# Kernel optimization log

Measured on AMD Instinct MI355X. Metric: run time of the kernel, lower is better.

Reference implementation:

```python
import jax, jax.numpy as jnp
import numpy as np

B, N = 16, 16          # batch, boxes per image
H, W = 640, 640        # image size
PH, PW = 300, 300      # learned patch size
MIN_AREA = 60.0
MAX_ANG = 20.0 * np.pi / 180.0


def setup_inputs() -> dict:
    key = jax.random.key(0)
    k1, k2, k3 = jax.random.split(key, 3)
    images = jax.random.uniform(k1, (B, H, W, 3), jnp.float32, -1.0, 1.0)
    patch = jax.random.uniform(k2, (PH, PW, 3), jnp.float32, -1.0, 1.0)
    kb1, kb2, kb3 = jax.random.split(k3, 3)
    ymin = jax.random.uniform(kb1, (B, N), jnp.float32, 0.0, H - 220.0)
    xmin = jax.random.uniform(kb2, (B, N), jnp.float32, 0.0, W - 220.0)
    hw = jax.random.uniform(kb3, (B, N, 2), jnp.float32, 100.0, 200.0)
    boxes = jnp.stack([ymin, xmin, ymin + hw[..., 0], xmin + hw[..., 1]], axis=-1)
    scale = jnp.float32(0.4)
    return {"boxes": boxes, "images": images, "patch": patch, "scale": scale}


def _bilinear(img, ys, xs):
    # img [Ph,Pw,3]; ys,xs [H,W] continuous source coords -> [H,W,3]
    Ph, Pw = img.shape[0], img.shape[1]
    y0 = jnp.floor(ys)
    x0 = jnp.floor(xs)
    wy = (ys - y0)[..., None]
    wx = (xs - x0)[..., None]
    y0i = jnp.clip(y0.astype(jnp.int32), 0, Ph - 1)
    y1i = jnp.clip(y0i + 1, 0, Ph - 1)
    x0i = jnp.clip(x0.astype(jnp.int32), 0, Pw - 1)
    x1i = jnp.clip(x0i + 1, 0, Pw - 1)
    v00 = img[y0i, x0i]
    v01 = img[y0i, x1i]
    v10 = img[y1i, x0i]
    v11 = img[y1i, x1i]
    return v00 * (1 - wy) * (1 - wx) + v01 * (1 - wy) * wx + v10 * wy * (1 - wx) + v11 * wy * wx


def _per_image(img, boxes_i, patch, scale, key):
    # random_print_adjust: per-channel affine jitter of the patch
    kw, kb, kloop = jax.random.split(key, 3)
    w = jax.random.normal(kw, (1, 1, 3), jnp.float32) * 0.1 + 0.5
    b = jax.random.normal(kb, (1, 1, 3), jnp.float32) * 0.01
    p = jnp.clip(w * patch + b, -1.0, 1.0)
    # BrightnessMatcher: shift patch mean brightness to match the image
    p = jnp.clip(p + (jnp.mean(img) - jnp.mean(p)), -1.0, 1.0)

    oimg = img
    mask0 = jnp.zeros_like(img)
    yy, xx = jnp.meshgrid(jnp.arange(H, dtype=jnp.float32),
                          jnp.arange(W, dtype=jnp.float32), indexing="ij")

    def step(carry, inp):
        image, mask = carry
        box, kk = inp
        ymin, xmin, ymax, xmax = box[0], box[1], box[2], box[3]
        h = ymax - ymin
        ww = xmax - xmin
        longer = jnp.maximum(h, ww)
        ps = jnp.floor(longer * scale)                       # patch_h == patch_w
        diag = jnp.minimum(jnp.sqrt(2.0).astype(jnp.float32) * ps, jnp.float32(W))
        oy = ymin + h / 2.0
        ox = xmin + ww / 2.0
        y0 = jnp.maximum(oy - diag / 2.0, 0.0)
        x0 = jnp.maximum(ox - diag / 2.0, 0.0)
        y0 = jnp.where(y0 + diag > H, H - diag, y0)
        x0 = jnp.where(x0 + diag > W, W - diag, x0)
        # int casts as in the TF code (values are >= 0, trunc == floor)
        y0i = jnp.floor(y0)
        x0i = jnp.floor(x0)
        phi = jnp.maximum(jnp.floor(ps), 1.0)
        diagi = jnp.floor(diag)
        valid_box = (phi * phi) > MIN_AREA

        k1, k2, k3 = jax.random.split(kk, 3)
        angle = jax.random.uniform(k1, (), jnp.float32, -MAX_ANG, MAX_ANG)

        # inverse warp: output pixel -> padded-patch coords -> resized-patch coords
        u = yy - y0i
        v = xx - x0i
        in_sq = (u >= 0) & (v >= 0) & (u < diagi) & (v < diagi)
        c = (diagi - 1.0) / 2.0
        ca, sa = jnp.cos(angle), jnp.sin(angle)
        su = c + ca * (u - c) - sa * (v - c)
        sv = c + sa * (u - c) + ca * (v - c)
        top = jnp.floor((diagi - phi) / 2.0)   # pad offset (floor top/left)
        py = su - top
        px = sv - top
        valid_src = (py >= 0) & (py <= phi - 1) & (px >= 0) & (px <= phi - 1)
        # resized-patch coords -> original patch coords (bilinear resize, half-pixel)
        sy = (py + 0.5) * (PH / phi) - 0.5
        sx = (px + 0.5) * (PW / phi) - 0.5
        samp = _bilinear(p, sy, sx)                                   # [H,W,3]
        noise = jax.random.uniform(k2, samp.shape, jnp.float32, -0.1, 0.1)
        bright = jax.random.uniform(k3, (), jnp.float32, -0.3, 0.3)
        im = jnp.clip(samp + noise + bright, -1.0, 1.0)
        val = jnp.where(valid_src[..., None], im, -2.0)
        val = jnp.where(val < -1.0, image, val)   # fill with current background
        val = jnp.clip(val, -1.0, 1.0)
        sel = (in_sq & valid_box)[..., None]
        new_image = jnp.where(sel, val, image)
        new_mask = jnp.where(sel, oimg - val, mask)
        return (new_image, new_mask), None

    keys = jax.random.split(kloop, N)
    (img_out, mask_out), _ = jax.lax.scan(step, (img, mask0), (boxes_i, keys))
    return img_out, mask_out


def reference(boxes, images, patch, scale):
    keys = jax.random.split(jax.random.key(42), B)
    img_out, mask_out = jax.vmap(_per_image, in_axes=(0, 0, None, None, 0))(
        images, boxes, patch, scale, keys)
    return img_out, mask_out
```

## Files before the change

### kernel.cpp

```cpp
#include <hip/hip_runtime.h>
#include <stdint.h>
#include <math.h>

#define B_ 16
#define N_ 16
#define H_ 640
#define W_ 640
#define PH_ 300
#define PW_ 300

#define IMG_ELEMS (H_*W_*3)
#define PATCH_ELEMS (PH_*PW_*3)

#define TROWS 16
#define TCOLS 64
#define TILES_Y (H_/TROWS)
#define TILES_X (W_/TCOLS)
#define TILES_PER_IMG (TILES_Y*TILES_X)

typedef float f32x4 __attribute__((ext_vector_type(4)));

__device__ __forceinline__ uint2 tf2x32(uint32_t k0, uint32_t k1, uint32_t x0, uint32_t x1) {
  uint32_t k2 = k0 ^ k1 ^ 0x1BD11BDAu;
#define TFR(r) x0 += x1; x1 = (x1 << (r)) | (x1 >> (32 - (r))); x1 ^= x0;
  x0 += k0; x1 += k1;
  TFR(13) TFR(15) TFR(26) TFR(6)
  x0 += k1; x1 += k2 + 1u;
  TFR(17) TFR(29) TFR(16) TFR(24)
  x0 += k2; x1 += k0 + 2u;
  TFR(13) TFR(15) TFR(26) TFR(6)
  x0 += k0; x1 += k1 + 3u;
  TFR(17) TFR(29) TFR(16) TFR(24)
  x0 += k1; x1 += k2 + 4u;
  TFR(13) TFR(15) TFR(26) TFR(6)
  x0 += k2; x1 += k0 + 5u;
#undef TFR
  return make_uint2(x0, x1);
}

__device__ __forceinline__ uint32_t rb32(uint32_t k0, uint32_t k1, uint32_t i) {
  uint2 o = tf2x32(k0, k1, 0u, i);
  return o.x ^ o.y;
}

__device__ __forceinline__ float u01f(uint32_t bits) {
  return __uint_as_float((bits >> 9) | 0x3F800000u) - 1.0f;
}

__device__ __forceinline__ float erfinv32(float x) {
  float w = -log1pf(-x * x);
  float p;
  if (w < 5.0f) {
    w = w - 2.5f;
    p = 2.81022636e-08f;
    p = fmaf(p, w, 3.43273939e-07f);
    p = fmaf(p, w, -3.5233877e-06f);
    p = fmaf(p, w, -4.39150654e-06f);
    p = fmaf(p, w, 0.00021858087f);
    p = fmaf(p, w, -0.00125372503f);
    p = fmaf(p, w, -0.00417768164f);
    p = fmaf(p, w, 0.246640727f);
    p = fmaf(p, w, 1.50140941f);
  } else {
    w = sqrtf(w) - 3.0f;
    p = -0.000200214257f;
    p = fmaf(p, w, 0.000100950558f);
    p = fmaf(p, w, 0.00134934322f);
    p = fmaf(p, w, -0.00367342844f);
    p = fmaf(p, w, 0.00573950773f);
    p = fmaf(p, w, -0.0076224613f);
    p = fmaf(p, w, 0.00943887047f);
    p = fmaf(p, w, 1.00167406f);
    p = fmaf(p, w, 2.83297682f);
  }
  return p * x;
}

__device__ __forceinline__ float jnormal(uint32_t bits) {
  float lo = __uint_as_float(0xBF7FFFFFu);
  float span = 1.0f - lo;
  float u = fmaxf(lo, u01f(bits) * span + lo);
  return 1.4142135623730951f * erfinv32(u);
}

__global__ void setup_kernel(const float* __restrict__ boxes, const float* __restrict__ scale_p,
                             float* __restrict__ params, float* __restrict__ wb) {
  int t = threadIdx.x;
  if (t >= B_*N_) return;
  int b = t >> 4, n = t & 15;
  uint2 kb = tf2x32(0u, 42u, 0u, (uint32_t)b);
  uint2 kw  = tf2x32(kb.x, kb.y, 0u, 0u);
  uint2 kbk = tf2x32(kb.x, kb.y, 0u, 1u);
  uint2 kl  = tf2x32(kb.x, kb.y, 0u, 2u);
  if (n == 0) {
    wb[b*8+0] = jnormal(rb32(kw.x,  kw.y,  0u)) * 0.1f + 0.5f;
    wb[b*8+1] = jnormal(rb32(kw.x,  kw.y,  1u)) * 0.1f + 0.5f;
    wb[b*8+2] = jnormal(rb32(kw.x,  kw.y,  2u)) * 0.1f + 0.5f;
    wb[b*8+3] = jnormal(rb32(kbk.x, kbk.y, 0u)) * 0.01f;
    wb[b*8+4] = jnormal(rb32(kbk.x, kbk.y, 1u)) * 0.01f;
    wb[b*8+5] = jnormal(rb32(kbk.x, kbk.y, 2u)) * 0.01f;
  }
  uint2 kk = tf2x32(kl.x, kl.y, 0u, (uint32_t)n);
  uint2 k1 = tf2x32(kk.x, kk.y, 0u, 0u);
  uint2 k2 = tf2x32(kk.x, kk.y, 0u, 1u);
  uint2 k3 = tf2x32(kk.x, kk.y, 0u, 2u);
  const float MA = (float)(20.0 * 3.14159265358979323846 / 180.0);
  float angle  = fmaxf(-MA,   u01f(rb32(k1.x, k1.y, 0u)) * (MA - (-MA)) + (-MA));
  float bright = fmaxf(-0.3f, u01f(rb32(k3.x, k3.y, 0u)) * (0.3f - (-0.3f)) + (-0.3f));

  const float* bx = boxes + (size_t)t * 4;
  float ymin = bx[0], xmin = bx[1], ymax = bx[2], xmax = bx[3];
  float sc = scale_p[0];
  float h = ymax - ymin, ww = xmax - xmin;
  float longer = fmaxf(h, ww);
  float ps = floorf(longer * sc);
  float diag = fminf(sqrtf(2.0f) * ps, (float)W_);
  float oy = ymin + h * 0.5f;
  float ox = xmin + ww * 0.5f;
  float y0 = fmaxf(oy - diag * 0.5f, 0.0f);
  float x0 = fmaxf(ox - diag * 0.5f, 0.0f);
  if (y0 + diag > (float)H_) y0 = (float)H_ - diag;
  if (x0 + diag > (float)W_) x0 = (float)W_ - diag;
  float y0i = floorf(y0), x0i = floorf(x0);
  float phi = fmaxf(floorf(ps), 1.0f);
  float diagi = floorf(diag);
  float validf = ((phi * phi) > 60.0f) ? 1.0f : 0.0f;
  float c = (diagi - 1.0f) * 0.5f;
  float top = floorf((diagi - phi) * 0.5f);

  float* P = params + t * 16;
  P[0] = y0i; P[1] = x0i; P[2] = diagi; P[3] = phi;
  P[4] = c;
  P[5] = (float)cos((double)angle);
  P[6] = (float)sin((double)angle);
  P[7] = top;
  P[8] = bright; P[9] = (float)PH_ / phi; P[10] = 0.0f; P[11] = validf;
  P[12] = __uint_as_float(k2.x); P[13] = __uint_as_float(k2.y); P[14] = 0.0f; P[15] = 0.0f;
}

__global__ __launch_bounds__(256) void reduce_kernel(
    const float* __restrict__ images, const float* __restrict__ patch,
    const float* __restrict__ wb, double* __restrict__ partials) {
  int b = blockIdx.y, j = blockIdx.x, t = threadIdx.x;
  const float* img = images + (size_t)b * IMG_ELEMS;
  double s = 0.0;
  for (int i = j * 256 + t; i < IMG_ELEMS; i += 64 * 256) s += (double)img[i];
  float w0 = wb[b*8+0], w1 = wb[b*8+1], w2 = wb[b*8+2];
  float b0 = wb[b*8+3], b1 = wb[b*8+4], b2 = wb[b*8+5];
  double sp = 0.0;
  for (int i = j * 256 + t; i < PATCH_ELEMS; i += 64 * 256) {
    int q = i / 3; int ch = i - q * 3;
    float wv = (ch == 0) ? w0 : ((ch == 1) ? w1 : w2);
    float bv = (ch == 0) ? b0 : ((ch == 1) ? b1 : b2);
    float pv = fminf(fmaxf(wv * patch[i] + bv, -1.0f), 1.0f);
    sp += (double)pv;
  }
  __shared__ double sh[256];
  sh[t] = s; __syncthreads();
  for (int o = 128; o > 0; o >>= 1) { if (t < o) sh[t] += sh[t + o]; __syncthreads(); }
  if (t == 0) partials[((size_t)b * 64 + j) * 2 + 0] = sh[0];
  __syncthreads();
  sh[t] = sp; __syncthreads();
  for (int o = 128; o > 0; o >>= 1) { if (t < o) sh[t] += sh[t + o]; __syncthreads(); }
  if (t == 0) partials[((size_t)b * 64 + j) * 2 + 1] = sh[0];
}

__global__ void finalize_kernel(const double* __restrict__ partials, float* __restrict__ dvals) {
  int t = threadIdx.x;
  if (t < B_) {
    double si = 0.0, sp = 0.0;
    for (int j = 0; j < 64; j++) {
      si += partials[((size_t)t * 64 + j) * 2 + 0];
      sp += partials[((size_t)t * 64 + j) * 2 + 1];
    }
    float mi = (float)(si / (double)IMG_ELEMS);
    float mp = (float)(sp / (double)PATCH_ELEMS);
    dvals[t] = mi - mp;
  }
}

__global__ __launch_bounds__(256) void patch_adjust_kernel(
    const float* __restrict__ patch, const float* __restrict__ wb,
    const float* __restrict__ dvals, float* __restrict__ padj) {
  int b = blockIdx.y;
  float w0 = wb[b*8+0], w1 = wb[b*8+1], w2 = wb[b*8+2];
  float b0 = wb[b*8+3], b1 = wb[b*8+4], b2 = wb[b*8+5];
  float dsh = dvals[b];
  float* dst = padj + (size_t)b * PATCH_ELEMS;
  int i0 = (blockIdx.x * 256 + threadIdx.x) * 4;
  if (i0 + 4 <= PATCH_ELEMS) {
    f32x4 pv = *(const f32x4*)(patch + i0);
    float o[4];
#pragma unroll
    for (int e = 0; e < 4; e++) {
      int ch = (i0 + e) % 3;
      float wv = (ch == 0) ? w0 : ((ch == 1) ? w1 : w2);
      float bv = (ch == 0) ? b0 : ((ch == 1) ? b1 : b2);
      float a = fminf(fmaxf(wv * pv[e] + bv, -1.0f), 1.0f);
      o[e] = fminf(fmaxf(a + dsh, -1.0f), 1.0f);
    }
    f32x4 ov = {o[0], o[1], o[2], o[3]};
    *(f32x4*)(dst + i0) = ov;
  }
}

template<int PADJ>
__global__ __launch_bounds__(256) void main_kernel(
    const float* __restrict__ images, const float* __restrict__ patchsrc,
    const float* __restrict__ params, const float* __restrict__ wb,
    const float* __restrict__ dvals, float* __restrict__ out) {
  __shared__ float sP[N_ * 16];
  __shared__ float sWB[6];
  __shared__ int sList[N_];
  __shared__ int sCount;
  __shared__ float sT[TROWS * 192];

  int bid = blockIdx.x;
  int b  = (bid & 7) * 2 + ((bid >> 3) & 1);
  int tl = bid >> 4;
  int ty = tl / TILES_X;
  int tx = tl - ty * TILES_X;
  int tid = threadIdx.x;

  if (tid < N_ * 16) sP[tid] = params[b * N_ * 16 + tid];
  if (PADJ == 0 && tid < 6) sWB[tid] = wb[b * 8 + tid];
  if (tid == 0) {
    const float* Pb = params + b * N_ * 16;
    float ys = (float)(ty * TROWS), ye = (float)(ty * TROWS + TROWS - 1);
    float xs = (float)(tx * TCOLS), xe = (float)(tx * TCOLS + TCOLS - 1);
    int cnt = 0;
    for (int n = 0; n < N_; n++) {
      const float* P = Pb + n * 16;
      if (P[11] == 0.0f) continue;
      float last = P[2] - 1.0f;
      if (P[0] + last < ys || P[0] > ye) continue;
      if (P[1] + last < xs || P[1] > xe) continue;
      sList[cnt++] = n;
    }
    sCount = cnt;
  }
  __syncthreads();

  int lane = tid & 63;
  int wv   = tid >> 6;
  size_t ibase = (size_t)b * IMG_ELEMS;
  size_t moff  = (size_t)B_ * IMG_ELEMS;

  int   ck[3], lrk[3];
  size_t fbk[3];
#pragma unroll
  for (int k = 0; k < 3; k++) {
    int t4 = k * 64 + lane;
    int r  = t4 / 48;
    int c  = t4 - r * 48;
    int lr = wv * 4 + r;
    ck[k] = c; lrk[k] = lr;
    fbk[k] = ibase + ((size_t)(ty * TROWS + lr) * W_ + tx * TCOLS) * 3 + (size_t)c * 4;
  }

  if (sCount == 0) {
    const f32x4 z = {0.0f, 0.0f, 0.0f, 0.0f};
#pragma unroll
    for (int k = 0; k < 3; k++) {
      f32x4 d = *(const f32x4*)(images + fbk[k]);
      __builtin_nontemporal_store(d, (f32x4*)(out + fbk[k]));
      __builtin_nontemporal_store(z, (f32x4*)(out + moff + fbk[k]));
    }
    return;
  }

  const float* patchb = PADJ ? (patchsrc + (size_t)b * PATCH_ELEMS) : patchsrc;
  float dsh = PADJ ? 0.0f : dvals[b];

#pragma unroll
  for (int k = 0; k < 3; k++) {
    f32x4 d = *(const f32x4*)(images + fbk[k]);
    *(f32x4*)(&sT[lrk[k] * 192 + ck[k] * 4]) = d;
  }

  int   pj[4];  float yfj[4];
  float xf = (float)(tx * TCOLS + lane);
#pragma unroll
  for (int j = 0; j < 4; j++) {
    int row = ty * TROWS + wv * 4 + j;
    pj[j]  = row * W_ + tx * TCOLS + lane;
    yfj[j] = (float)row;
  }

  float orig[12], img[12], mkv[12];
#pragma unroll
  for (int j = 0; j < 4; j++) {
    int base = (wv * 4 + j) * 192 + lane * 3;
    orig[j*3+0] = sT[base + 0];
    orig[j*3+1] = sT[base + 1];
    orig[j*3+2] = sT[base + 2];
  }
#pragma unroll
  for (int e = 0; e < 12; e++) { img[e] = orig[e]; mkv[e] = 0.0f; }

  int cnt = sCount;
  for (int li = 0; li < cnt; li++) {
    const float* P = sP + sList[li] * 16;
    float P0 = P[0], P1 = P[1], diagi = P[2];
    float phi = P[3], c = P[4], ca = P[5], sa = P[6], top = P[7], bright = P[8], sph = P[9];
    uint32_t k2a = __float_as_uint(P[12]);
    uint32_t k2b = __float_as_uint(P[13]);
    float v = xf - P1;
    bool vok = (v >= 0.0f && v < diagi);
    float t2 = v - c;
#pragma unroll
    for (int j = 0; j < 4; j++) {
      float u = yfj[j] - P0;
      if (!(u >= 0.0f && u < diagi)) continue;
      if (!vok) continue;
      float t1 = u - c;
      float su = (c + ca * t1) - sa * t2;
      float sv = (c + sa * t1) + ca * t2;
      float py = su - top;
      float px = sv - top;
      bool vsrc = (py >= 0.0f) && (py <= phi - 1.0f) && (px >= 0.0f) && (px <= phi - 1.0f);
      if (vsrc) {
        float sy = (py + 0.5f) * sph - 0.5f;
        float sx = (px + 0.5f) * sph - 0.5f;
        float fy = floorf(sy), fx = floorf(sx);
        float wy = sy - fy, wxv = sx - fx;
        int iy0 = min(max((int)fy, 0), PH_ - 1);
        int iy1 = min(iy0 + 1, PH_ - 1);
        int ix0 = min(max((int)fx, 0), PW_ - 1);
        int ix1 = min(ix0 + 1, PW_ - 1);
        int o00 = (iy0 * PW_ + ix0) * 3;
        int o01 = (iy0 * PW_ + ix1) * 3;
        int o10 = (iy1 * PW_ + ix0) * 3;
        int o11 = (iy1 * PW_ + ix1) * 3;
        float omwy = 1.0f - wy, omwx = 1.0f - wxv;
        int nbase = pj[j] * 3;
#pragma unroll
        for (int ch = 0; ch < 3; ch++) {
          float a00, a01, a10, a11;
          if (PADJ) {
            a00 = patchb[o00 + ch];
            a01 = patchb[o01 + ch];
            a10 = patchb[o10 + ch];
            a11 = patchb[o11 + ch];
          } else {
            float wv2 = sWB[ch], bv = sWB[3 + ch];
            a00 = fminf(fmaxf(wv2 * patchb[o00 + ch] + bv, -1.0f), 1.0f);
            a01 = fminf(fmaxf(wv2 * patchb[o01 + ch] + bv, -1.0f), 1.0f);
            a10 = fminf(fmaxf(wv2 * patchb[o10 + ch] + bv, -1.0f), 1.0f);
            a11 = fminf(fmaxf(wv2 * patchb[o11 + ch] + bv, -1.0f), 1.0f);
            a00 = fminf(fmaxf(a00 + dsh, -1.0f), 1.0f);
            a01 = fminf(fmaxf(a01 + dsh, -1.0f), 1.0f);
            a10 = fminf(fmaxf(a10 + dsh, -1.0f), 1.0f);
            a11 = fminf(fmaxf(a11 + dsh, -1.0f), 1.0f);
          }
          float samp = ((a00 * omwy) * omwx) + ((a01 * omwy) * wxv)
                     + ((a10 * wy) * omwx) + ((a11 * wy) * wxv);
          uint32_t bits = rb32(k2a, k2b, (uint32_t)(nbase + ch));
          float nz = fmaxf(-0.1f, u01f(bits) * (0.1f - (-0.1f)) + (-0.1f));
          float imv = fminf(fmaxf((samp + nz) + bright, -1.0f), 1.0f);
          img[j * 3 + ch] = imv;
          mkv[j * 3 + ch] = orig[j * 3 + ch] - imv;
        }
      } else {
#pragma unroll
        for (int ch = 0; ch < 3; ch++) mkv[j * 3 + ch] = orig[j * 3 + ch] - img[j * 3 + ch];
      }
    }
  }

#pragma unroll
  for (int j = 0; j < 4; j++) {
    int base = (wv * 4 + j) * 192 + lane * 3;
    sT[base + 0] = img[j*3+0];
    sT[base + 1] = img[j*3+1];
    sT[base + 2] = img[j*3+2];
  }
#pragma unroll
  for (int k = 0; k < 3; k++) {
    f32x4 d = *(const f32x4*)(&sT[lrk[k] * 192 + ck[k] * 4]);
    __builtin_nontemporal_store(d, (f32x4*)(out + fbk[k]));
  }
#pragma unroll
  for (int j = 0; j < 4; j++) {
    int base = (wv * 4 + j) * 192 + lane * 3;
    sT[base + 0] = mkv[j*3+0];
    sT[base + 1] = mkv[j*3+1];
    sT[base + 2] = mkv[j*3+2];
  }
#pragma unroll
  for (int k = 0; k < 3; k++) {
    f32x4 d = *(const f32x4*)(&sT[lrk[k] * 192 + ck[k] * 4]);
    __builtin_nontemporal_store(d, (f32x4*)(out + moff + fbk[k]));
  }
}

extern "C" void kernel_launch(void* const* d_in, const int* in_sizes, int n_in,
                              void* d_out, int out_size, void* d_ws, size_t ws_size,
                              hipStream_t stream) {
  const float* boxes  = (const float*)d_in[0];
  const float* images = (const float*)d_in[1];
  const float* patch  = (const float*)d_in[2];
  const float* scale  = (const float*)d_in[3];
  float* out = (float*)d_out;

  float* params = (float*)d_ws;
  float* wb     = params + B_ * N_ * 16;
  float* dvals  = wb + B_ * 8;
  double* partials = (double*)((char*)d_ws + 20480);
  float* padj   = (float*)((char*)d_ws + 36864);
  const size_t PADJ_NEED = 36864 + (size_t)B_ * PATCH_ELEMS * 4;

  setup_kernel<<<1, 256, 0, stream>>>(boxes, scale, params, wb);
  reduce_kernel<<<dim3(64, B_), 256, 0, stream>>>(images, patch, wb, partials);
  finalize_kernel<<<1, 64, 0, stream>>>(partials, dvals);
  if (ws_size >= PADJ_NEED) {
    patch_adjust_kernel<<<dim3((PATCH_ELEMS + 1023) / 1024, B_), 256, 0, stream>>>(
        patch, wb, dvals, padj);
    main_kernel<1><<<B_ * TILES_PER_IMG, 256, 0, stream>>>(
        images, padj, params, wb, dvals, out);
  } else {
    main_kernel<0><<<B_ * TILES_PER_IMG, 256, 0, stream>>>(
        images, patch, params, wb, dvals, out);
  }
}
```

Baseline: 292.6 us.

## Precompute tile box masks and split copy and paint tiles into separate kernels

A new cull kernel computes a per-tile bitmask of boxes that overlap each tile. A separate copy kernel handles the tiles with no boxes, and the paint kernel reads the mask and loops over set bits instead of building a list serially in thread 0. This removes the per-block serial cull and the barrier stall, and keeps the paint kernel's register and LDS footprint away from the pure-copy tiles. In exchange it adds two extra kernel launches and two full grids of mostly early-exiting blocks.

Result: slower. 309.1 us (+5.6%).

```diff
diff --git a/kernel.cpp b/kernel.cpp
--- a/kernel.cpp
+++ b/kernel.cpp
@@ -17,6 +17,7 @@
 #define TILES_Y (H_/TROWS)
 #define TILES_X (W_/TCOLS)
 #define TILES_PER_IMG (TILES_Y*TILES_X)
+#define NTILES (B_*TILES_PER_IMG)
 
 typedef float f32x4 __attribute__((ext_vector_type(4)));
 
@@ -138,6 +139,29 @@
   P[12] = __uint_as_float(k2.x); P[13] = __uint_as_float(k2.y); P[14] = 0.0f; P[15] = 0.0f;
 }
 
+__global__ __launch_bounds__(256) void cull_kernel(const float* __restrict__ params,
+                                                   uint32_t* __restrict__ tilemask) {
+  int t = blockIdx.x * 256 + threadIdx.x;
+  if (t >= NTILES) return;
+  int b  = (t & 7) * 2 + ((t >> 3) & 1);
+  int tl = t >> 4;
+  int ty = tl / TILES_X;
+  int tx = tl - ty * TILES_X;
+  const float* Pb = params + b * N_ * 16;
+  float ys = (float)(ty * TROWS), ye = (float)(ty * TROWS + TROWS - 1);
+  float xs = (float)(tx * TCOLS), xe = (float)(tx * TCOLS + TCOLS - 1);
+  uint32_t m = 0;
+  for (int n = 0; n < N_; n++) {
+    const float* P = Pb + n * 16;
+    if (P[11] == 0.0f) continue;
+    float last = P[2] - 1.0f;
+    if (P[0] + last < ys || P[0] > ye) continue;
+    if (P[1] + last < xs || P[1] > xe) continue;
+    m |= (1u << n);
+  }
+  tilemask[t] = m;
+}
+
 __global__ __launch_bounds__(256) void reduce_kernel(
     const float* __restrict__ images, const float* __restrict__ patch,
     const float* __restrict__ wb, double* __restrict__ partials) {
@@ -204,47 +228,64 @@
   }
 }
 
-template<int PADJ>
-__global__ __launch_bounds__(256) void main_kernel(
-    const float* __restrict__ images, const float* __restrict__ patchsrc,
-    const float* __restrict__ params, const float* __restrict__ wb,
-    const float* __restrict__ dvals, float* __restrict__ out) {
-  __shared__ float sP[N_ * 16];
-  __shared__ float sWB[6];
-  __shared__ int sList[N_];
-  __shared__ int sCount;
-  __shared__ float sT[TROWS * 192];
-
+__global__ __launch_bounds__(256) void copy_kernel(
+    const float* __restrict__ images, const uint32_t* __restrict__ tilemask,
+    float* __restrict__ out) {
   int bid = blockIdx.x;
+  if (tilemask[bid] != 0u) return;
   int b  = (bid & 7) * 2 + ((bid >> 3) & 1);
   int tl = bid >> 4;
   int ty = tl / TILES_X;
   int tx = tl - ty * TILES_X;
   int tid = threadIdx.x;
-
-  if (tid < N_ * 16) sP[tid] = params[b * N_ * 16 + tid];
-  if (PADJ == 0 && tid < 6) sWB[tid] = wb[b * 8 + tid];
-  if (tid == 0) {
-    const float* Pb = params + b * N_ * 16;
-    float ys = (float)(ty * TROWS), ye = (float)(ty * TROWS + TROWS - 1);
-    float xs = (float)(tx * TCOLS), xe = (float)(tx * TCOLS + TCOLS - 1);
-    int cnt = 0;
-    for (int n = 0; n < N_; n++) {
-      const float* P = Pb + n * 16;
-      if (P[11] == 0.0f) continue;
-      float last = P[2] - 1.0f;
-      if (P[0] + last < ys || P[0] > ye) continue;
-      if (P[1] + last < xs || P[1] > xe) continue;
-      sList[cnt++] = n;
-    }
-    sCount = cnt;
-  }
-  __syncthreads();
-
   int lane = tid & 63;
   int wv   = tid >> 6;
   size_t ibase = (size_t)b * IMG_ELEMS;
   size_t moff  = (size_t)B_ * IMG_ELEMS;
+  const f32x4 z = {0.0f, 0.0f, 0.0f, 0.0f};
+#pragma unroll
+  for (int k = 0; k < 3; k++) {
+    int t4 = k * 64 + lane;
+    int r  = t4 / 48;
+    int c  = t4 - r * 48;
+    int row = ty * TROWS + wv * 4 + r;
+    size_t fb = ibase + ((size_t)row * W_ + tx * TCOLS) * 3 + (size_t)c * 4;
+    f32x4 d = *(const f32x4*)(images + fb);
+    __builtin_nontemporal_store(d, (f32x4*)(out + fb));
+    __builtin_nontemporal_store(z, (f32x4*)(out + moff + fb));
+  }
+}
+
+template<int PADJ>
+__global__ __launch_bounds__(256) void paint_kernel(
+    const float* __restrict__ images, const float* __restrict__ patchsrc,
+    const float* __restrict__ params, const float* __restrict__ wb,
+    const float* __restrict__ dvals, const uint32_t* __restrict__ tilemask,
+    float* __restrict__ out) {
+  __shared__ float sP[N_ * 16];
+  __shared__ float sWB[6];
+  __shared__ float sT[TROWS * 192];
+
+  int bid = blockIdx.x;
+  uint32_t mask = tilemask[bid];
+  if (mask == 0u) return;
+  int b  = (bid & 7) * 2 + ((bid >> 3) & 1);
+  int tl = bid >> 4;
+  int ty = tl / TILES_X;
+  int tx = tl - ty * TILES_X;
+  int tid = threadIdx.x;
+
+  if (tid < N_ * 16) sP[tid] = params[b * N_ * 16 + tid];
+  if (PADJ == 0 && tid < 6) sWB[tid] = wb[b * 8 + tid];
+  __syncthreads();
+
+  int lane = tid & 63;
+  int wv   = tid >> 6;
+  size_t ibase = (size_t)b * IMG_ELEMS;
+  size_t moff  = (size_t)B_ * IMG_ELEMS;
+
+  const float* patchb = PADJ ? (patchsrc + (size_t)b * PATCH_ELEMS) : patchsrc;
+  float dsh = PADJ ? 0.0f : dvals[b];
 
   int   ck[3], lrk[3];
   size_t fbk[3];
@@ -256,26 +297,8 @@
     int lr = wv * 4 + r;
     ck[k] = c; lrk[k] = lr;
     fbk[k] = ibase + ((size_t)(ty * TROWS + lr) * W_ + tx * TCOLS) * 3 + (size_t)c * 4;
-  }
-
-  if (sCount == 0) {
-    const f32x4 z = {0.0f, 0.0f, 0.0f, 0.0f};
-#pragma unroll
-    for (int k = 0; k < 3; k++) {
-      f32x4 d = *(const f32x4*)(images + fbk[k]);
-      __builtin_nontemporal_store(d, (f32x4*)(out + fbk[k]));
-      __builtin_nontemporal_store(z, (f32x4*)(out + moff + fbk[k]));
-    }
-    return;
-  }
-
-  const float* patchb = PADJ ? (patchsrc + (size_t)b * PATCH_ELEMS) : patchsrc;
-  float dsh = PADJ ? 0.0f : dvals[b];
-
-#pragma unroll
-  for (int k = 0; k < 3; k++) {
     f32x4 d = *(const f32x4*)(images + fbk[k]);
-    *(f32x4*)(&sT[lrk[k] * 192 + ck[k] * 4]) = d;
+    *(f32x4*)(&sT[lr * 192 + c * 4]) = d;
   }
 
   int   pj[4];  float yfj[4];
@@ -298,9 +321,11 @@
 #pragma unroll
   for (int e = 0; e < 12; e++) { img[e] = orig[e]; mkv[e] = 0.0f; }
 
-  int cnt = sCount;
-  for (int li = 0; li < cnt; li++) {
-    const float* P = sP + sList[li] * 16;
+  uint32_t m = mask;
+  while (m) {
+    int n = __builtin_ctz(m);
+    m &= m - 1u;
+    const float* P = sP + n * 16;
     float P0 = P[0], P1 = P[1], diagi = P[2];
     float phi = P[3], c = P[4], ca = P[5], sa = P[6], top = P[7], bright = P[8], sph = P[9];
     uint32_t k2a = __float_as_uint(P[12]);
@@ -406,20 +431,23 @@
   float* params = (float*)d_ws;
   float* wb     = params + B_ * N_ * 16;
   float* dvals  = wb + B_ * 8;
-  double* partials = (double*)((char*)d_ws + 20480);
-  float* padj   = (float*)((char*)d_ws + 36864);
-  const size_t PADJ_NEED = 36864 + (size_t)B_ * PATCH_ELEMS * 4;
+  uint32_t* tilemask = (uint32_t*)((char*)d_ws + 17408);
+  double* partials   = (double*)((char*)d_ws + 43008);
+  float* padj        = (float*)((char*)d_ws + 59392);
+  const size_t PADJ_NEED = 59392 + (size_t)B_ * PATCH_ELEMS * 4;
 
   setup_kernel<<<1, 256, 0, stream>>>(boxes, scale, params, wb);
+  cull_kernel<<<(NTILES + 255) / 256, 256, 0, stream>>>(params, tilemask);
   reduce_kernel<<<dim3(64, B_), 256, 0, stream>>>(images, patch, wb, partials);
   finalize_kernel<<<1, 64, 0, stream>>>(partials, dvals);
+  copy_kernel<<<NTILES, 256, 0, stream>>>(images, tilemask, out);
   if (ws_size >= PADJ_NEED) {
     patch_adjust_kernel<<<dim3((PATCH_ELEMS + 1023) / 1024, B_), 256, 0, stream>>>(
         patch, wb, dvals, padj);
-    main_kernel<1><<<B_ * TILES_PER_IMG, 256, 0, stream>>>(
-        images, padj, params, wb, dvals, out);
+    paint_kernel<1><<<NTILES, 256, 0, stream>>>(
+        images, padj, params, wb, dvals, tilemask, out);
   } else {
-    main_kernel<0><<<B_ * TILES_PER_IMG, 256, 0, stream>>>(
-        images, patch, params, wb, dvals, out);
-  }
-}
+    paint_kernel<0><<<NTILES, 256, 0, stream>>>(
+        images, patch, params, wb, dvals, tilemask, out);
+  }
+}
```
